# Performance work log

Measured on AMD Instinct MI355X. Metric: run time of the kernel, lower is better.

## Reference

```python
import jax, jax.numpy as jnp
import numpy as np

D = 2048          # lstm_size
V = 4096          # uniform num_tokens for all 5 decision groups
NUM_LAYERS = 4    # len(num_tokens) - 1 loop iterations; one final decode after


def setup_inputs() -> dict:
    key = jax.random.key(0)
    ks = jax.random.split(key, 10)
    s = 0.02
    n = lambda k, shape: jax.random.normal(k, shape, dtype=jnp.float32) * s
    return {
        "emb0": n(ks[0], (1, D)),                 # Embedding(1, D) initial input
        "w_ih": n(ks[1], (4 * D, D)),             # LSTMCell input weights (i,f,g,o)
        "w_hh": n(ks[2], (4 * D, D)),
        "b_ih": jnp.zeros((4 * D,), jnp.float32),
        "b_hh": jnp.zeros((4 * D,), jnp.float32),
        "lin1_w": n(ks[3], (D, D)),
        "lin1_b": jnp.zeros((D,), jnp.float32),
        "lin2_w": n(ks[4], (D, D)),
        "lin2_b": jnp.zeros((D,), jnp.float32),
        "lin3_w": n(ks[5], (1, D)),
        "lin3_b": jnp.zeros((1,), jnp.float32),
        "dec_w": n(ks[6], (5, V, D)),             # 5 decoders Linear(D, V)
        "dec_b": jnp.zeros((5, V), jnp.float32),
        "emb_tables": n(ks[7], (4, V, D)),        # only embeddings[0..3] are used
    }


def _lstm_cell(x, h, c, w_ih, w_hh, b_ih, b_hh):
    # torch.nn.LSTMCell math; gate order i, f, g, o
    gates = x @ w_ih.T + b_ih + h @ w_hh.T + b_hh
    i, f, g, o = jnp.split(gates, 4, axis=-1)
    i, f, o = jax.nn.sigmoid(i), jax.nn.sigmoid(f), jax.nn.sigmoid(o)
    g = jnp.tanh(g)
    c_new = f * c + i * g
    h_new = o * jnp.tanh(c_new)
    return h_new, c_new


def reference(emb0, w_ih, w_hh, b_ih, b_hh, lin1_w, lin1_b, lin2_w, lin2_b,
              lin3_w, lin3_b, dec_w, dec_b, emb_tables):
    key = jax.random.key(42)
    step = 0

    def sample(logits, step):
        # stable softmax stats computed once via log_softmax
        logp = jax.nn.log_softmax(logits, axis=-1)
        p = jnp.exp(logp)
        ent = -(logp * p).sum(1)                              # (1,)
        idx = jax.random.categorical(jax.random.fold_in(key, step), logits, axis=-1)  # (1,)
        sel_lp = jnp.take_along_axis(logp, idx[:, None], axis=1).squeeze(1)           # (1,)
        return idx, sel_lp, jax.lax.stop_gradient(ent)

    # NOTE: source names the LSTMCell outputs (next_c, next_h) = lstm(...),
    # i.e. swapped vs torch's (h, c). State threading stays consistent, but all
    # downstream linears/decoders/all_h consume the CELL state c. Reproduced here.
    h = jnp.zeros((1, D), jnp.float32)
    c = jnp.zeros((1, D), jnp.float32)
    inputs = emb0
    all_c, all_cw = [], []
    arc, lps, ents = [], [], []

    for layer_id in range(NUM_LAYERS):
        h, c = _lstm_cell(inputs, h, c, w_ih, w_hh, b_ih, b_hh)
        all_c.append(c)
        all_cw.append(c @ lin1_w.T + lin1_b)
        query = jnp.tanh((c @ lin2_w.T + lin2_b) + jnp.concatenate(all_cw, 0))  # (layer_id+1, D)
        logits = (query @ lin3_w.T + lin3_b).reshape(1, layer_id + 1)
        skip_idx, lp, en = sample(logits, step); step += 1
        arc.append(skip_idx); lps.append(lp); ents.append(en)
        inputs = jnp.concatenate(all_c, 0)[skip_idx]            # (1, D)

        h, c = _lstm_cell(inputs, h, c, w_ih, w_hh, b_ih, b_hh)
        logits = c @ dec_w[layer_id].T + dec_b[layer_id]        # (1, V)
        func, lp, en = sample(logits, step); step += 1
        arc.append(func); lps.append(lp); ents.append(en)
        inputs = emb_tables[layer_id][func]                     # (1, D)

    # final model decision
    h, c = _lstm_cell(inputs, h, c, w_ih, w_hh, b_ih, b_hh)
    logits = c @ dec_w[-1].T + dec_b[-1]
    func, lp, en = sample(logits, step)
    arc.append(func); lps.append(lp); ents.append(en)

    arc_seq = jnp.concatenate(arc, 0)            # (9,) int32
    sample_entropy = jnp.concatenate(ents, 0)    # (9,)
    sample_log_probs = jnp.concatenate(lps, 0)   # (9,)
    return arc_seq, sample_entropy, sample_log_probs
```

## Files before the change

kernel.cpp:

```cpp
#include <hip/hip_runtime.h>
#include <stdint.h>

#define D 2048
#define V 4096
#define TINYF 1.17549435e-38f
#define NINF (-__builtin_huge_valf())

#if __has_builtin(__builtin_amdgcn_cvt_pk_f32_fp8) && __has_builtin(__builtin_amdgcn_cvt_pk_fp8_f32)
#define HWFP8 1
#define POSTSCALE 0.015625f
#else
#define HWFP8 0
#define POSTSCALE 1.52587890625e-05f
#endif

typedef float vfloat2 __attribute__((ext_vector_type(2)));
typedef float vfloat4 __attribute__((ext_vector_type(4)));

__device__ __forceinline__ void tf_block(uint32_t k0, uint32_t k1, uint32_t x0, uint32_t x1,
                                         uint32_t& o0, uint32_t& o1) {
  uint32_t ks2 = k0 ^ k1 ^ 0x1BD11BDAu;
  uint32_t ks[3] = {k0, k1, ks2};
  x0 += k0; x1 += k1;
  const uint32_t rotA[4] = {13u, 15u, 26u, 6u};
  const uint32_t rotB[4] = {17u, 29u, 16u, 24u};
#pragma unroll
  for (int i = 0; i < 5; ++i) {
    const uint32_t* rot = (i & 1) ? rotB : rotA;
#pragma unroll
    for (int j = 0; j < 4; ++j) {
      uint32_t r = rot[j];
      x0 += x1;
      x1 = (x1 << r) | (x1 >> (32u - r));
      x1 ^= x0;
    }
    x0 += ks[(i + 1) % 3];
    x1 += ks[(i + 2) % 3] + (uint32_t)(i + 1);
  }
  o0 = x0; o1 = x1;
}

__device__ __forceinline__ float gumbel_at(uint32_t k1, uint32_t k2, int i) {
  uint32_t o0, o1;
  tf_block(k1, k2, 0u, (uint32_t)i, o0, o1);
  uint32_t bits = o0 ^ o1;
  float u = __uint_as_float((bits >> 9) | 0x3F800000u) - 1.0f;
  u = fmaxf(TINYF, u + TINYF);
  return -logf(-logf(u));
}

#if !HWFP8
__device__ __forceinline__ float dec1(uint32_t v) {
  uint32_t e = (v >> 3) & 15u, m = v & 7u;
  int K = e ? (int)((8u + m) << e) : (int)(m << 1);
  float f = (float)K;
  return (v & 0x80u) ? -f : f;
}
__device__ __forceinline__ uint32_t enc1(float xf) {
  uint32_t b = __float_as_uint(xf);
  uint32_t s = (b >> 24) & 0x80u;
  float ax = fabsf(xf);
  if (ax < 0.015625f) return s | (uint32_t)(int)rintf(ax * 512.f);
  uint32_t ab = b & 0x7FFFFFFFu;
  ab += 0x7FFFFu + ((ab >> 20) & 1u);
  int e = (int)(ab >> 23) - 120;
  uint32_t m = (ab >> 20) & 7u;
  if (e < 1) return s | (uint32_t)(int)rintf(ax * 512.f);
  if (e > 15) { e = 15; m = 7u; }
  return s | ((uint32_t)e << 3) | m;
}
#endif

__device__ __forceinline__ void dec8(uint2 u, float* w) {
#if HWFP8
  vfloat2 a = __builtin_amdgcn_cvt_pk_f32_fp8((int)u.x, false);
  vfloat2 b = __builtin_amdgcn_cvt_pk_f32_fp8((int)u.x, true);
  vfloat2 c = __builtin_amdgcn_cvt_pk_f32_fp8((int)u.y, false);
  vfloat2 d = __builtin_amdgcn_cvt_pk_f32_fp8((int)u.y, true);
  w[0] = a.x; w[1] = a.y; w[2] = b.x; w[3] = b.y;
  w[4] = c.x; w[5] = c.y; w[6] = d.x; w[7] = d.y;
#else
  uint32_t p = u.x, q = u.y;
  w[0] = dec1(p & 255u); w[1] = dec1((p >> 8) & 255u);
  w[2] = dec1((p >> 16) & 255u); w[3] = dec1(p >> 24);
  w[4] = dec1(q & 255u); w[5] = dec1((q >> 8) & 255u);
  w[6] = dec1((q >> 16) & 255u); w[7] = dec1(q >> 24);
#endif
}

__device__ __forceinline__ float4 ntload4(const float4* p) {
  vfloat4 v = __builtin_nontemporal_load((const vfloat4*)p);
  return make_float4(v.x, v.y, v.z, v.w);
}

__device__ __forceinline__ float row_dot8(const uint8_t* __restrict__ row,
                                          const float* __restrict__ xs, int lane) {
  float a = 0.f;
#pragma unroll
  for (int k = lane * 8; k < D; k += 512) {
    uint2 u = *(const uint2*)(row + k);
    float w[8]; dec8(u, w);
    float4 x0 = *(const float4*)(xs + k);
    float4 x1 = *(const float4*)(xs + k + 4);
    a += w[0] * x0.x + w[1] * x0.y + w[2] * x0.z + w[3] * x0.w
       + w[4] * x1.x + w[5] * x1.y + w[6] * x1.z + w[7] * x1.w;
  }
  return a;
}

__global__ __launch_bounds__(256) void convert_k(const float* __restrict__ wih,
                                                 const float* __restrict__ whh,
                                                 const float* __restrict__ l1,
                                                 const float* __restrict__ l2,
                                                 uint8_t* __restrict__ dw) {
  size_t gid = (size_t)blockIdx.x * 256 + threadIdx.x;
  const size_t C1 = (size_t)4 * D * D / 8;
  const size_t C2 = 2 * C1;
  const size_t C3 = C2 + (size_t)D * D / 8;
  const size_t C4 = C3 + (size_t)D * D / 8;
  const float* src; size_t off, dbase;
  if (gid < C1)      { src = wih; off = gid;      dbase = 0; }
  else if (gid < C2) { src = whh; off = gid - C1; dbase = (size_t)4 * D * D; }
  else if (gid < C3) { src = l1;  off = gid - C2; dbase = (size_t)8 * D * D; }
  else if (gid < C4) { src = l2;  off = gid - C3; dbase = (size_t)9 * D * D; }
  else return;
  const float4* s = (const float4*)(src + off * 8);
  float4 a = ntload4(s), b = ntload4(s + 1);
  float v[8] = {a.x * 64.f, a.y * 64.f, a.z * 64.f, a.w * 64.f,
                b.x * 64.f, b.y * 64.f, b.z * 64.f, b.w * 64.f};
  uint2 o;
#if HWFP8
  int lo = __builtin_amdgcn_cvt_pk_fp8_f32(v[0], v[1], 0, false);
  lo     = __builtin_amdgcn_cvt_pk_fp8_f32(v[2], v[3], lo, true);
  int hi = __builtin_amdgcn_cvt_pk_fp8_f32(v[4], v[5], 0, false);
  hi     = __builtin_amdgcn_cvt_pk_fp8_f32(v[6], v[7], hi, true);
  o.x = (uint32_t)lo; o.y = (uint32_t)hi;
#else
  o.x = enc1(v[0]) | (enc1(v[1]) << 8) | (enc1(v[2]) << 16) | (enc1(v[3]) << 24);
  o.y = enc1(v[4]) | (enc1(v[5]) << 8) | (enc1(v[6]) << 16) | (enc1(v[7]) << 24);
#endif
  *(uint2*)(dw + dbase + off * 8) = o;
}

template <bool SAMPLE>
__global__ __launch_bounds__(256) void lstm_cell_k(
    const uint8_t* __restrict__ w_ih, const uint8_t* __restrict__ w_hh,
    const float* __restrict__ b_ih, const float* __restrict__ b_hh,
    const float* __restrict__ x_base, const float* __restrict__ logits, int step,
    const float* __restrict__ h_in, const float* __restrict__ c_in,
    float* __restrict__ h_out, float* __restrict__ c_out, float* __restrict__ c_copy,
    float* __restrict__ out_arc, float* __restrict__ out_ent, float* __restrict__ out_lp) {
  __shared__ float xs[D];
  __shared__ float hs[D];
  __shared__ float red[256];
  __shared__ int redi[256];
  __shared__ int s_sel;
  int tid = threadIdx.x;
  const float* x = x_base;
  if (SAMPLE) {
    uint32_t k1, k2; tf_block(0u, 42u, 0u, (uint32_t)step, k1, k2);
    float xv[16];
    float m = NINF, bv = NINF; int bi = 1 << 30;
#pragma unroll
    for (int t = 0; t < 16; ++t) {
      int i = tid + t * 256;
      float xl = logits[i];
      xv[t] = xl;
      m = fmaxf(m, xl);
      float sc = gumbel_at(k1, k2, i) + xl;
      if (sc > bv) { bv = sc; bi = i; }
    }
    red[tid] = m; __syncthreads();
    for (int st = 128; st; st >>= 1) { if (tid < st) red[tid] = fmaxf(red[tid], red[tid + st]); __syncthreads(); }
    m = red[0]; __syncthreads();
    float S = 0.f, T = 0.f;
#pragma unroll
    for (int t = 0; t < 16; ++t) { float e = expf(xv[t] - m); S += e; T += e * (xv[t] - m); }
    red[tid] = S; __syncthreads();
    for (int st = 128; st; st >>= 1) { if (tid < st) red[tid] += red[tid + st]; __syncthreads(); }
    S = red[0]; __syncthreads();
    red[tid] = T; __syncthreads();
    for (int st = 128; st; st >>= 1) { if (tid < st) red[tid] += red[tid + st]; __syncthreads(); }
    T = red[0]; __syncthreads();
    red[tid] = bv; redi[tid] = bi; __syncthreads();
    for (int st = 128; st; st >>= 1) {
      if (tid < st) {
        float ov = red[tid + st]; int oi = redi[tid + st];
        if (ov > red[tid] || (ov == red[tid] && oi < redi[tid])) { red[tid] = ov; redi[tid] = oi; }
      }
      __syncthreads();
    }
    if (tid == 0) {
      int idx = redi[0];
      s_sel = idx;
      if (blockIdx.x == 0) {
        float L = logf(S);
        *out_arc = (float)idx;
        *out_ent = L - T / S;
        *out_lp  = logits[idx] - m - L;
      }
    }
    __syncthreads();
    x = x_base + (size_t)s_sel * D;
  }
  for (int i = tid; i < D; i += 256) { xs[i] = x[i]; hs[i] = h_in ? h_in[i] : 0.f; }
  __syncthreads();
  int wave = tid >> 6, lane = tid & 63;
  int j = blockIdx.x * 4 + wave;
  float gv[4];
#pragma unroll
  for (int m4 = 0; m4 < 4; ++m4) {
    float a = row_dot8(w_ih + (size_t)(m4 * D + j) * D, xs, lane)
            + row_dot8(w_hh + (size_t)(m4 * D + j) * D, hs, lane);
#pragma unroll
    for (int off = 32; off > 0; off >>= 1) a += __shfl_down(a, off, 64);
    gv[m4] = a * POSTSCALE + b_ih[m4 * D + j] + b_hh[m4 * D + j];
  }
  if (lane == 0) {
    float ig = 1.f / (1.f + expf(-gv[0]));
    float fg = 1.f / (1.f + expf(-gv[1]));
    float gg = tanhf(gv[2]);
    float og = 1.f / (1.f + expf(-gv[3]));
    float ci = c_in ? c_in[j] : 0.f;
    float cn = fg * ci + ig * gg;
    float hn = og * tanhf(cn);
    c_out[j] = cn;
    h_out[j] = hn;
    if (c_copy) c_copy[j] = cn;
  }
}

template <int NC>
__global__ __launch_bounds__(256) void spec_lin_k(
    const uint8_t* __restrict__ w_ih, const uint8_t* __restrict__ w_hh,
    const float* __restrict__ b_ih, const float* __restrict__ b_hh,
    const float* __restrict__ h1, const float* __restrict__ all_c,
    const uint8_t* __restrict__ l1w, const float* __restrict__ l1b,
    const uint8_t* __restrict__ l2w, const float* __restrict__ l2b,
    const float* __restrict__ c1,
    float* __restrict__ g_ih, float* __restrict__ g_hh,
    float* __restrict__ cw_dst, float* __restrict__ qb) {
  __shared__ float xs[D];
  int tid = threadIdx.x;
  int wave = tid >> 6, lane = tid & 63;
  int b = blockIdx.x;
  if (b < 512) {
    int j = b * 4 + wave;
    float acc[4][NC + 1];
#pragma unroll
    for (int m = 0; m < 4; ++m)
#pragma unroll
      for (int t = 0; t < NC + 1; ++t) acc[m][t] = 0.f;
    for (int k = lane * 8; k < D; k += 512) {
      float xh[8];
      float xc[NC][8];
      *(float4*)xh       = *(const float4*)(h1 + k);
      *(float4*)(xh + 4) = *(const float4*)(h1 + k + 4);
#pragma unroll
      for (int t = 0; t < NC; ++t) {
        *(float4*)(xc[t])     = *(const float4*)(all_c + (size_t)t * D + k);
        *(float4*)(xc[t] + 4) = *(const float4*)(all_c + (size_t)t * D + k + 4);
      }
#pragma unroll
      for (int m = 0; m < 4; ++m) {
        float wi[8], wh[8];
        dec8(*(const uint2*)(w_ih + (size_t)(m * D + j) * D + k), wi);
        dec8(*(const uint2*)(w_hh + (size_t)(m * D + j) * D + k), wh);
#pragma unroll
        for (int e = 0; e < 8; ++e) acc[m][0] += wh[e] * xh[e];
#pragma unroll
        for (int t = 0; t < NC; ++t)
#pragma unroll
          for (int e = 0; e < 8; ++e) acc[m][1 + t] += wi[e] * xc[t][e];
      }
    }
#pragma unroll
    for (int m = 0; m < 4; ++m)
#pragma unroll
      for (int t = 0; t < NC + 1; ++t) {
        float a = acc[m][t];
#pragma unroll
        for (int o = 32; o > 0; o >>= 1) a += __shfl_down(a, o, 64);
        if (lane == 0) {
          if (t == 0) g_hh[m * D + j] = a * POSTSCALE + b_ih[m * D + j] + b_hh[m * D + j];
          else        g_ih[((size_t)(t - 1) * 4 + m) * D + j] = a * POSTSCALE;
        }
      }
  } else {
    for (int i = tid; i < D; i += 256) xs[i] = c1[i];
    __syncthreads();
    int b2 = b - 512;
    const uint8_t* Wp; const float* bp; float* dst; int row;
    if (b2 < 512) { row = b2 * 4 + wave; Wp = l1w; bp = l1b; dst = cw_dst; }
    else          { row = (b2 - 512) * 4 + wave; Wp = l2w; bp = l2b; dst = qb; }
    float a = row_dot8(Wp + (size_t)row * D, xs, lane);
#pragma unroll
    for (int o = 32; o > 0; o >>= 1) a += __shfl_down(a, o, 64);
    if (lane == 0) dst[row] = a * POSTSCALE + bp[row];
  }
}

__global__ __launch_bounds__(256) void dec_fused_k(
    const float* __restrict__ Wdec, const float* __restrict__ bdec,
    const float* __restrict__ g_ih, const float* __restrict__ g_hh,
    const float* __restrict__ c1,
    const float* __restrict__ qb, const float* __restrict__ all_cw,
    const float* __restrict__ lin3_w, const float* __restrict__ lin3_b,
    int ncand, int step,
    float* __restrict__ logits,
    float* __restrict__ h2_out, float* __restrict__ c2_out,
    float* __restrict__ out_arc, float* __restrict__ out_ent, float* __restrict__ out_lp) {
  __shared__ float xs[D];
  __shared__ float red[16];
  __shared__ int s_sel;
  int tid = threadIdx.x, wave = tid >> 6, lane = tid & 63;
  for (int t = 0; t < ncand; ++t) {
    float s = 0.f;
    for (int k = tid; k < D; k += 256) s += tanhf(qb[k] + all_cw[(size_t)t * D + k]) * lin3_w[k];
#pragma unroll
    for (int o = 32; o > 0; o >>= 1) s += __shfl_down(s, o, 64);
    if (lane == 0) red[t * 4 + wave] = s;
  }
  __syncthreads();
  if (tid == 0) {
    float sl[4];
    for (int t = 0; t < ncand; ++t)
      sl[t] = red[t * 4] + red[t * 4 + 1] + red[t * 4 + 2] + red[t * 4 + 3] + lin3_b[0];
    uint32_t k1, k2; tf_block(0u, 42u, 0u, (uint32_t)step, k1, k2);
    float m = NINF;
    for (int i = 0; i < ncand; ++i) m = fmaxf(m, sl[i]);
    float S = 0.f, T = 0.f;
    for (int i = 0; i < ncand; ++i) { float e = expf(sl[i] - m); S += e; T += e * (sl[i] - m); }
    float L = logf(S);
    float bv = NINF; int bi = 0;
    for (int i = 0; i < ncand; ++i) {
      float sc = gumbel_at(k1, k2, i) + sl[i];
      if (sc > bv) { bv = sc; bi = i; }
    }
    s_sel = bi;
    if (blockIdx.x == 0) {
      *out_arc = (float)bi;
      *out_ent = L - T / S;
      *out_lp  = sl[bi] - m - L;
    }
  }
  __syncthreads();
  int sel = s_sel;
  const float* gi = g_ih + (size_t)sel * 4 * D;
  bool b0 = (blockIdx.x == 0);
  for (int j = tid; j < D; j += 256) {
    float gI = gi[j]         + g_hh[j];
    float gF = gi[D + j]     + g_hh[D + j];
    float gG = gi[2 * D + j] + g_hh[2 * D + j];
    float gO = gi[3 * D + j] + g_hh[3 * D + j];
    float ig = 1.f / (1.f + expf(-gI));
    float fg = 1.f / (1.f + expf(-gF));
    float gg = tanhf(gG);
    float og = 1.f / (1.f + expf(-gO));
    float cn = fg * c1[j] + ig * gg;
    xs[j] = cn;
    if (b0) { c2_out[j] = cn; h2_out[j] = og * tanhf(cn); }
  }
  __syncthreads();
  int row = blockIdx.x * 4 + wave;
  const float* wr = Wdec + (size_t)row * D;
  float a = 0.f;
#pragma unroll
  for (int k = lane * 4; k < D; k += 256) {
    float4 w = ntload4((const float4*)(wr + k));
    float4 x = *(const float4*)(xs + k);
    a += w.x * x.x + w.y * x.y + w.z * x.z + w.w * x.w;
  }
#pragma unroll
  for (int o = 32; o > 0; o >>= 1) a += __shfl_down(a, o, 64);
  if (lane == 0) logits[row] = a + bdec[row];
}

__global__ __launch_bounds__(256) void gemv_k(const float* __restrict__ W,
                                              const float* __restrict__ bias,
                                              const float* __restrict__ c,
                                              float* __restrict__ y) {
  __shared__ float xs[D];
  int tid = threadIdx.x;
  for (int i = tid; i < D; i += 256) xs[i] = c[i];
  __syncthreads();
  int wave = tid >> 6, lane = tid & 63;
  int row = blockIdx.x * 4 + wave;
  const float* wr = W + (size_t)row * D;
  float a = 0.f;
#pragma unroll
  for (int k = lane * 4; k < D; k += 256) {
    float4 w = ntload4((const float4*)(wr + k));
    float4 x = *(const float4*)(xs + k);
    a += w.x * x.x + w.y * x.y + w.z * x.z + w.w * x.w;
  }
#pragma unroll
  for (int o = 32; o > 0; o >>= 1) a += __shfl_down(a, o, 64);
  if (lane == 0) y[row] = a + bias[row];
}

__global__ __launch_bounds__(1024) void sample_k(const float* __restrict__ logits, int step,
                                                 float* __restrict__ out_arc,
                                                 float* __restrict__ out_ent,
                                                 float* __restrict__ out_lp,
                                                 int* __restrict__ sel_out) {
  __shared__ float red[1024];
  __shared__ int redi[1024];
  int tid = threadIdx.x;
  uint32_t k1, k2; tf_block(0u, 42u, 0u, (uint32_t)step, k1, k2);
  float xv[4];
  float m = NINF, bv = NINF; int bi = 1 << 30;
#pragma unroll
  for (int t = 0; t < 4; ++t) {
    int i = tid + t * 1024;
    float x = logits[i];
    xv[t] = x;
    m = fmaxf(m, x);
    float sc = gumbel_at(k1, k2, i) + x;
    if (sc > bv) { bv = sc; bi = i; }
  }
  red[tid] = m; __syncthreads();
  for (int st = 512; st; st >>= 1) { if (tid < st) red[tid] = fmaxf(red[tid], red[tid + st]); __syncthreads(); }
  m = red[0]; __syncthreads();
  float S = 0.f, T = 0.f;
#pragma unroll
  for (int t = 0; t < 4; ++t) { float e = expf(xv[t] - m); S += e; T += e * (xv[t] - m); }
  red[tid] = S; __syncthreads();
  for (int st = 512; st; st >>= 1) { if (tid < st) red[tid] += red[tid + st]; __syncthreads(); }
  S = red[0]; __syncthreads();
  red[tid] = T; __syncthreads();
  for (int st = 512; st; st >>= 1) { if (tid < st) red[tid] += red[tid + st]; __syncthreads(); }
  T = red[0]; __syncthreads();
  red[tid] = bv; redi[tid] = bi; __syncthreads();
  for (int st = 512; st; st >>= 1) {
    if (tid < st) {
      float ov = red[tid + st]; int oi = redi[tid + st];
      if (ov > red[tid] || (ov == red[tid] && oi < redi[tid])) { red[tid] = ov; redi[tid] = oi; }
    }
    __syncthreads();
  }
  if (tid == 0) {
    float L = logf(S);
    int idx = redi[0];
    *out_arc = (float)idx;
    *out_ent = L - T / S;
    *out_lp  = logits[idx] - m - L;
    *sel_out = idx;
  }
}

extern "C" void kernel_launch(void* const* d_in, const int* in_sizes, int n_in,
                              void* d_out, int out_size, void* d_ws, size_t ws_size,
                              hipStream_t stream) {
  const float* emb0   = (const float*)d_in[0];
  const float* w_ih   = (const float*)d_in[1];
  const float* w_hh   = (const float*)d_in[2];
  const float* b_ih   = (const float*)d_in[3];
  const float* b_hh   = (const float*)d_in[4];
  const float* lin1_w = (const float*)d_in[5];
  const float* lin1_b = (const float*)d_in[6];
  const float* lin2_w = (const float*)d_in[7];
  const float* lin2_b = (const float*)d_in[8];
  const float* lin3_w = (const float*)d_in[9];
  const float* lin3_b = (const float*)d_in[10];
  const float* dec_w  = (const float*)d_in[11];
  const float* dec_b  = (const float*)d_in[12];
  const float* embt   = (const float*)d_in[13];

  float* out = (float*)d_out;
  float* ws = (float*)d_ws;

  float* hA     = ws;
  float* cA     = ws + D;
  float* hB     = ws + 2 * D;
  float* cB     = ws + 3 * D;
  float* all_c  = ws + 4 * D;
  float* all_cw = ws + 8 * D;
  float* qb     = ws + 12 * D;
  float* logits = ws + 13 * D;
  int* sel_d    = (int*)(ws + 15 * D);
  float* g_hh   = ws + 16 * D;
  float* g_ih   = ws + 20 * D;
  uint8_t* w8   = (uint8_t*)(ws + 36 * D);
  uint8_t* wih8 = w8;
  uint8_t* whh8 = w8 + (size_t)4 * D * D;
  uint8_t* l18  = w8 + (size_t)8 * D * D;
  uint8_t* l28  = w8 + (size_t)9 * D * D;

  convert_k<<<20480, 256, 0, stream>>>(w_ih, w_hh, lin1_w, lin2_w, w8);

  auto launch_spec = [&](int layer) {
    float* cw = all_cw + (size_t)layer * D;
    switch (layer) {
      case 0:  spec_lin_k<1><<<1536, 256, 0, stream>>>(wih8, whh8, b_ih, b_hh, hA, all_c, l18, lin1_b, l28, lin2_b, cA, g_ih, g_hh, cw, qb); break;
      case 1:  spec_lin_k<2><<<1536, 256, 0, stream>>>(wih8, whh8, b_ih, b_hh, hA, all_c, l18, lin1_b, l28, lin2_b, cA, g_ih, g_hh, cw, qb); break;
      case 2:  spec_lin_k<3><<<1536, 256, 0, stream>>>(wih8, whh8, b_ih, b_hh, hA, all_c, l18, lin1_b, l28, lin2_b, cA, g_ih, g_hh, cw, qb); break;
      default: spec_lin_k<4><<<1536, 256, 0, stream>>>(wih8, whh8, b_ih, b_hh, hA, all_c, l18, lin1_b, l28, lin2_b, cA, g_ih, g_hh, cw, qb); break;
    }
  };

  for (int layer = 0; layer < 4; ++layer) {
    float* ccopy = all_c + (size_t)layer * D;
    if (layer == 0) {
      lstm_cell_k<false><<<512, 256, 0, stream>>>(wih8, whh8, b_ih, b_hh,
                                                  emb0, nullptr, 0,
                                                  nullptr, nullptr, hA, cA, ccopy,
                                                  nullptr, nullptr, nullptr);
    } else {
      int ps = 2 * layer - 1;
      lstm_cell_k<true><<<512, 256, 0, stream>>>(wih8, whh8, b_ih, b_hh,
                                                 embt + (size_t)(layer - 1) * V * D,
                                                 logits, ps,
                                                 hB, cB, hA, cA, ccopy,
                                                 out + ps, out + 9 + ps, out + 18 + ps);
    }
    launch_spec(layer);
    int step = 2 * layer;
    dec_fused_k<<<V / 4, 256, 0, stream>>>(dec_w + (size_t)layer * V * D,
                                           dec_b + (size_t)layer * V,
                                           g_ih, g_hh, cA, qb, all_cw, lin3_w, lin3_b,
                                           layer + 1, step, logits, hB, cB,
                                           out + step, out + 9 + step, out + 18 + step);
  }

  lstm_cell_k<true><<<512, 256, 0, stream>>>(wih8, whh8, b_ih, b_hh,
                                             embt + (size_t)3 * V * D, logits, 7,
                                             hB, cB, hA, cA, nullptr,
                                             out + 7, out + 16, out + 25);
  gemv_k<<<V / 4, 256, 0, stream>>>(dec_w + (size_t)4 * V * D, dec_b + (size_t)4 * V,
                                    cA, logits);
  sample_k<<<1, 1024, 0, stream>>>(logits, 8, out + 8, out + 17, out + 26, sel_d);
}
```

Baseline: 282.4 us.

## Fuse fp8 weight conversion into first use and precompute sampling partials

Drops the separate conversion kernel. The first LSTM cell and the first spec_lin pass now read the fp32 weights, compute the dot product in full precision, and write the fp8 copy as a side effect. The decoder GEMV kernels also emit per-block softmax/Gumbel partials (max, sum, entropy term, best score and index), so each sampling LSTM block and the final sampler only merge 1024 partials instead of rescanning all 4096 logits. This removes a full extra pass over the weights and repeated per-block Gumbel/exp work. The trade-off is that the first step uses fp32 weights, which differs numerically from the quantized path, and the partial merges use a rescaled online-softmax combine.

```diff
diff --git a/kernel.cpp b/kernel.cpp
--- a/kernel.cpp
+++ b/kernel.cpp
@@ -88,46 +88,7 @@
 #endif
 }
 
-__device__ __forceinline__ float4 ntload4(const float4* p) {
-  vfloat4 v = __builtin_nontemporal_load((const vfloat4*)p);
-  return make_float4(v.x, v.y, v.z, v.w);
-}
-
-__device__ __forceinline__ float row_dot8(const uint8_t* __restrict__ row,
-                                          const float* __restrict__ xs, int lane) {
-  float a = 0.f;
-#pragma unroll
-  for (int k = lane * 8; k < D; k += 512) {
-    uint2 u = *(const uint2*)(row + k);
-    float w[8]; dec8(u, w);
-    float4 x0 = *(const float4*)(xs + k);
-    float4 x1 = *(const float4*)(xs + k + 4);
-    a += w[0] * x0.x + w[1] * x0.y + w[2] * x0.z + w[3] * x0.w
-       + w[4] * x1.x + w[5] * x1.y + w[6] * x1.z + w[7] * x1.w;
-  }
-  return a;
-}
-
-__global__ __launch_bounds__(256) void convert_k(const float* __restrict__ wih,
-                                                 const float* __restrict__ whh,
-                                                 const float* __restrict__ l1,
-                                                 const float* __restrict__ l2,
-                                                 uint8_t* __restrict__ dw) {
-  size_t gid = (size_t)blockIdx.x * 256 + threadIdx.x;
-  const size_t C1 = (size_t)4 * D * D / 8;
-  const size_t C2 = 2 * C1;
-  const size_t C3 = C2 + (size_t)D * D / 8;
-  const size_t C4 = C3 + (size_t)D * D / 8;
-  const float* src; size_t off, dbase;
-  if (gid < C1)      { src = wih; off = gid;      dbase = 0; }
-  else if (gid < C2) { src = whh; off = gid - C1; dbase = (size_t)4 * D * D; }
-  else if (gid < C3) { src = l1;  off = gid - C2; dbase = (size_t)8 * D * D; }
-  else if (gid < C4) { src = l2;  off = gid - C3; dbase = (size_t)9 * D * D; }
-  else return;
-  const float4* s = (const float4*)(src + off * 8);
-  float4 a = ntload4(s), b = ntload4(s + 1);
-  float v[8] = {a.x * 64.f, a.y * 64.f, a.z * 64.f, a.w * 64.f,
-                b.x * 64.f, b.y * 64.f, b.z * 64.f, b.w * 64.f};
+__device__ __forceinline__ uint2 enc8(const float* v) {
   uint2 o;
 #if HWFP8
   int lo = __builtin_amdgcn_cvt_pk_fp8_f32(v[0], v[1], 0, false);
@@ -139,69 +100,130 @@
   o.x = enc1(v[0]) | (enc1(v[1]) << 8) | (enc1(v[2]) << 16) | (enc1(v[3]) << 24);
   o.y = enc1(v[4]) | (enc1(v[5]) << 8) | (enc1(v[6]) << 16) | (enc1(v[7]) << 24);
 #endif
-  *(uint2*)(dw + dbase + off * 8) = o;
-}
-
-template <bool SAMPLE>
+  return o;
+}
+
+__device__ __forceinline__ float4 ntload4(const float4* p) {
+  vfloat4 v = __builtin_nontemporal_load((const vfloat4*)p);
+  return make_float4(v.x, v.y, v.z, v.w);
+}
+
+__device__ __forceinline__ float row_dot8(const uint8_t* __restrict__ row,
+                                          const float* __restrict__ xs, int lane) {
+  float a = 0.f;
+#pragma unroll
+  for (int k = lane * 8; k < D; k += 512) {
+    uint2 u = *(const uint2*)(row + k);
+    float w[8]; dec8(u, w);
+    float4 x0 = *(const float4*)(xs + k);
+    float4 x1 = *(const float4*)(xs + k + 4);
+    a += w[0] * x0.x + w[1] * x0.y + w[2] * x0.z + w[3] * x0.w
+       + w[4] * x1.x + w[5] * x1.y + w[6] * x1.z + w[7] * x1.w;
+  }
+  return a;
+}
+
+__device__ __forceinline__ float row_dot_conv(const float* __restrict__ row,
+                                              const float* __restrict__ xs, int lane,
+                                              uint8_t* __restrict__ out8) {
+  float a = 0.f;
+#pragma unroll
+  for (int k = lane * 8; k < D; k += 512) {
+    float4 w0 = ntload4((const float4*)(row + k));
+    float4 w1 = ntload4((const float4*)(row + k + 4));
+    float4 x0 = *(const float4*)(xs + k);
+    float4 x1 = *(const float4*)(xs + k + 4);
+    a += w0.x * x0.x + w0.y * x0.y + w0.z * x0.z + w0.w * x0.w
+       + w1.x * x1.x + w1.y * x1.y + w1.z * x1.z + w1.w * x1.w;
+    float v[8] = {w0.x * 64.f, w0.y * 64.f, w0.z * 64.f, w0.w * 64.f,
+                  w1.x * 64.f, w1.y * 64.f, w1.z * 64.f, w1.w * 64.f};
+    *(uint2*)(out8 + k) = enc8(v);
+  }
+  return a;
+}
+
+struct SampPart { float m, S, T, bv; int bi; };
+
+__device__ __forceinline__ void merge_part(SampPart& a, float qm, float qS, float qT,
+                                           float qb, int qi) {
+  float nm = fmaxf(a.m, qm);
+  float ea = expf(a.m - nm), eq = expf(qm - nm);
+  a.T = (a.T + (a.m - nm) * a.S) * ea + (qT + (qm - nm) * qS) * eq;
+  a.S = a.S * ea + qS * eq;
+  a.m = nm;
+  if (qb > a.bv || (qb == a.bv && qi < a.bi)) { a.bv = qb; a.bi = qi; }
+}
+
+__device__ __forceinline__ SampPart reduce_parts(const float4* __restrict__ part4,
+                                                 const int* __restrict__ parti,
+                                                 float* rm, float* rS, float* rT,
+                                                 float* rb, int* ri, int tid) {
+  float4 p = part4[4 * tid];
+  SampPart a = {p.x, p.y, p.z, p.w, parti[4 * tid]};
+#pragma unroll
+  for (int r = 1; r < 4; ++r) {
+    float4 q = part4[4 * tid + r];
+    merge_part(a, q.x, q.y, q.z, q.w, parti[4 * tid + r]);
+  }
+  rm[tid] = a.m; rS[tid] = a.S; rT[tid] = a.T; rb[tid] = a.bv; ri[tid] = a.bi;
+  __syncthreads();
+  for (int st = 128; st; st >>= 1) {
+    if (tid < st) {
+      merge_part(a, rm[tid + st], rS[tid + st], rT[tid + st], rb[tid + st], ri[tid + st]);
+      rm[tid] = a.m; rS[tid] = a.S; rT[tid] = a.T; rb[tid] = a.bv; ri[tid] = a.bi;
+    }
+    __syncthreads();
+  }
+  SampPart res = {rm[0], rS[0], rT[0], rb[0], ri[0]};
+  __syncthreads();
+  return res;
+}
+
+__device__ __forceinline__ void block_partial(const float* sl4, int base, int step,
+                                              float4* __restrict__ part4,
+                                              int* __restrict__ parti, int blk) {
+  uint32_t k1, k2; tf_block(0u, 42u, 0u, (uint32_t)step, k1, k2);
+  float x0 = sl4[0], x1 = sl4[1], x2 = sl4[2], x3 = sl4[3];
+  float pm = fmaxf(fmaxf(x0, x1), fmaxf(x2, x3));
+  float e0 = expf(x0 - pm), e1 = expf(x1 - pm), e2 = expf(x2 - pm), e3 = expf(x3 - pm);
+  float pS = e0 + e1 + e2 + e3;
+  float pT = e0 * (x0 - pm) + e1 * (x1 - pm) + e2 * (x2 - pm) + e3 * (x3 - pm);
+  float pb = NINF; int pbi = base;
+  float g;
+  g = gumbel_at(k1, k2, base + 0) + x0; if (g > pb) { pb = g; pbi = base + 0; }
+  g = gumbel_at(k1, k2, base + 1) + x1; if (g > pb) { pb = g; pbi = base + 1; }
+  g = gumbel_at(k1, k2, base + 2) + x2; if (g > pb) { pb = g; pbi = base + 2; }
+  g = gumbel_at(k1, k2, base + 3) + x3; if (g > pb) { pb = g; pbi = base + 3; }
+  part4[blk] = make_float4(pm, pS, pT, pb);
+  parti[blk] = pbi;
+}
+
+template <bool CONV, bool SAMPLE>
 __global__ __launch_bounds__(256) void lstm_cell_k(
-    const uint8_t* __restrict__ w_ih, const uint8_t* __restrict__ w_hh,
+    const void* __restrict__ w_ih_v, const void* __restrict__ w_hh_v,
+    uint8_t* __restrict__ wih8_out, uint8_t* __restrict__ whh8_out,
     const float* __restrict__ b_ih, const float* __restrict__ b_hh,
-    const float* __restrict__ x_base, const float* __restrict__ logits, int step,
+    const float* __restrict__ x_base,
+    const float4* __restrict__ part4, const int* __restrict__ parti,
+    const float* __restrict__ logits,
     const float* __restrict__ h_in, const float* __restrict__ c_in,
     float* __restrict__ h_out, float* __restrict__ c_out, float* __restrict__ c_copy,
     float* __restrict__ out_arc, float* __restrict__ out_ent, float* __restrict__ out_lp) {
   __shared__ float xs[D];
   __shared__ float hs[D];
-  __shared__ float red[256];
-  __shared__ int redi[256];
-  __shared__ int s_sel;
+  __shared__ float rm[256], rS[256], rT[256], rb[256];
+  __shared__ int ri[256];
   int tid = threadIdx.x;
   const float* x = x_base;
   if (SAMPLE) {
-    uint32_t k1, k2; tf_block(0u, 42u, 0u, (uint32_t)step, k1, k2);
-    float xv[16];
-    float m = NINF, bv = NINF; int bi = 1 << 30;
-#pragma unroll
-    for (int t = 0; t < 16; ++t) {
-      int i = tid + t * 256;
-      float xl = logits[i];
-      xv[t] = xl;
-      m = fmaxf(m, xl);
-      float sc = gumbel_at(k1, k2, i) + xl;
-      if (sc > bv) { bv = sc; bi = i; }
-    }
-    red[tid] = m; __syncthreads();
-    for (int st = 128; st; st >>= 1) { if (tid < st) red[tid] = fmaxf(red[tid], red[tid + st]); __syncthreads(); }
-    m = red[0]; __syncthreads();
-    float S = 0.f, T = 0.f;
-#pragma unroll
-    for (int t = 0; t < 16; ++t) { float e = expf(xv[t] - m); S += e; T += e * (xv[t] - m); }
-    red[tid] = S; __syncthreads();
-    for (int st = 128; st; st >>= 1) { if (tid < st) red[tid] += red[tid + st]; __syncthreads(); }
-    S = red[0]; __syncthreads();
-    red[tid] = T; __syncthreads();
-    for (int st = 128; st; st >>= 1) { if (tid < st) red[tid] += red[tid + st]; __syncthreads(); }
-    T = red[0]; __syncthreads();
-    red[tid] = bv; redi[tid] = bi; __syncthreads();
-    for (int st = 128; st; st >>= 1) {
-      if (tid < st) {
-        float ov = red[tid + st]; int oi = redi[tid + st];
-        if (ov > red[tid] || (ov == red[tid] && oi < redi[tid])) { red[tid] = ov; redi[tid] = oi; }
-      }
-      __syncthreads();
-    }
-    if (tid == 0) {
-      int idx = redi[0];
-      s_sel = idx;
-      if (blockIdx.x == 0) {
-        float L = logf(S);
-        *out_arc = (float)idx;
-        *out_ent = L - T / S;
-        *out_lp  = logits[idx] - m - L;
-      }
-    }
-    __syncthreads();
-    x = x_base + (size_t)s_sel * D;
+    SampPart g = reduce_parts(part4, parti, rm, rS, rT, rb, ri, tid);
+    if (tid == 0 && blockIdx.x == 0) {
+      float L = logf(g.S);
+      *out_arc = (float)g.bi;
+      *out_ent = L - g.T / g.S;
+      *out_lp  = logits[g.bi] - g.m - L;
+    }
+    x = x_base + (size_t)g.bi * D;
   }
   for (int i = tid; i < D; i += 256) { xs[i] = x[i]; hs[i] = h_in ? h_in[i] : 0.f; }
   __syncthreads();
@@ -210,11 +232,19 @@
   float gv[4];
 #pragma unroll
   for (int m4 = 0; m4 < 4; ++m4) {
-    float a = row_dot8(w_ih + (size_t)(m4 * D + j) * D, xs, lane)
-            + row_dot8(w_hh + (size_t)(m4 * D + j) * D, hs, lane);
+    size_t roff = (size_t)(m4 * D + j) * D;
+    float a;
+    if (CONV) {
+      a = row_dot_conv((const float*)w_ih_v + roff, xs, lane, wih8_out + roff)
+        + row_dot_conv((const float*)w_hh_v + roff, hs, lane, whh8_out + roff);
+    } else {
+      a = row_dot8((const uint8_t*)w_ih_v + roff, xs, lane)
+        + row_dot8((const uint8_t*)w_hh_v + roff, hs, lane);
+      a *= POSTSCALE;
+    }
 #pragma unroll
     for (int off = 32; off > 0; off >>= 1) a += __shfl_down(a, off, 64);
-    gv[m4] = a * POSTSCALE + b_ih[m4 * D + j] + b_hh[m4 * D + j];
+    gv[m4] = a + b_ih[m4 * D + j] + b_hh[m4 * D + j];
   }
   if (lane == 0) {
     float ig = 1.f / (1.f + expf(-gv[0]));
@@ -230,13 +260,14 @@
   }
 }
 
-template <int NC>
+template <int NC, bool CONV>
 __global__ __launch_bounds__(256) void spec_lin_k(
     const uint8_t* __restrict__ w_ih, const uint8_t* __restrict__ w_hh,
     const float* __restrict__ b_ih, const float* __restrict__ b_hh,
     const float* __restrict__ h1, const float* __restrict__ all_c,
-    const uint8_t* __restrict__ l1w, const float* __restrict__ l1b,
-    const uint8_t* __restrict__ l2w, const float* __restrict__ l2b,
+    const void* __restrict__ l1_v, const float* __restrict__ l1b,
+    const void* __restrict__ l2_v, const float* __restrict__ l2b,
+    uint8_t* __restrict__ l18_out, uint8_t* __restrict__ l28_out,
     const float* __restrict__ c1,
     float* __restrict__ g_ih, float* __restrict__ g_hh,
     float* __restrict__ cw_dst, float* __restrict__ qb) {
@@ -290,13 +321,16 @@
     for (int i = tid; i < D; i += 256) xs[i] = c1[i];
     __syncthreads();
     int b2 = b - 512;
-    const uint8_t* Wp; const float* bp; float* dst; int row;
-    if (b2 < 512) { row = b2 * 4 + wave; Wp = l1w; bp = l1b; dst = cw_dst; }
-    else          { row = (b2 - 512) * 4 + wave; Wp = l2w; bp = l2b; dst = qb; }
-    float a = row_dot8(Wp + (size_t)row * D, xs, lane);
+    const void* Wp; const float* bp; float* dst; uint8_t* o8; int row;
+    if (b2 < 512) { row = b2 * 4 + wave; Wp = l1_v; bp = l1b; dst = cw_dst; o8 = l18_out; }
+    else          { row = (b2 - 512) * 4 + wave; Wp = l2_v; bp = l2b; dst = qb; o8 = l28_out; }
+    size_t roff = (size_t)row * D;
+    float a;
+    if (CONV) a = row_dot_conv((const float*)Wp + roff, xs, lane, o8 + roff);
+    else      a = row_dot8((const uint8_t*)Wp + roff, xs, lane) * POSTSCALE;
 #pragma unroll
     for (int o = 32; o > 0; o >>= 1) a += __shfl_down(a, o, 64);
-    if (lane == 0) dst[row] = a * POSTSCALE + bp[row];
+    if (lane == 0) dst[row] = a + bp[row];
   }
 }
 
@@ -309,9 +343,11 @@
     int ncand, int step,
     float* __restrict__ logits,
     float* __restrict__ h2_out, float* __restrict__ c2_out,
-    float* __restrict__ out_arc, float* __restrict__ out_ent, float* __restrict__ out_lp) {
+    float* __restrict__ out_arc, float* __restrict__ out_ent, float* __restrict__ out_lp,
+    float4* __restrict__ part4, int* __restrict__ parti) {
   __shared__ float xs[D];
   __shared__ float red[16];
+  __shared__ float sl4[4];
   __shared__ int s_sel;
   int tid = threadIdx.x, wave = tid >> 6, lane = tid & 63;
   for (int t = 0; t < ncand; ++t) {
@@ -373,14 +409,17 @@
   }
 #pragma unroll
   for (int o = 32; o > 0; o >>= 1) a += __shfl_down(a, o, 64);
-  if (lane == 0) logits[row] = a + bdec[row];
-}
-
-__global__ __launch_bounds__(256) void gemv_k(const float* __restrict__ W,
-                                              const float* __restrict__ bias,
-                                              const float* __restrict__ c,
-                                              float* __restrict__ y) {
+  if (lane == 0) { float lv = a + bdec[row]; logits[row] = lv; sl4[wave] = lv; }
+  __syncthreads();
+  if (tid == 0) block_partial(sl4, blockIdx.x * 4, step + 1, part4, parti, blockIdx.x);
+}
+
+__global__ __launch_bounds__(256) void gemv_k(
+    const float* __restrict__ W, const float* __restrict__ bias,
+    const float* __restrict__ c, float* __restrict__ y, int step,
+    float4* __restrict__ part4, int* __restrict__ parti) {
   __shared__ float xs[D];
+  __shared__ float sl4[4];
   int tid = threadIdx.x;
   for (int i = tid; i < D; i += 256) xs[i] = c[i];
   __syncthreads();
@@ -396,56 +435,24 @@
   }
 #pragma unroll
   for (int o = 32; o > 0; o >>= 1) a += __shfl_down(a, o, 64);
-  if (lane == 0) y[row] = a + bias[row];
-}
-
-__global__ __launch_bounds__(1024) void sample_k(const float* __restrict__ logits, int step,
-                                                 float* __restrict__ out_arc,
-                                                 float* __restrict__ out_ent,
-                                                 float* __restrict__ out_lp,
-                                                 int* __restrict__ sel_out) {
-  __shared__ float red[1024];
-  __shared__ int redi[1024];
+  if (lane == 0) { float lv = a + bias[row]; y[row] = lv; sl4[wave] = lv; }
+  __syncthreads();
+  if (tid == 0) block_partial(sl4, blockIdx.x * 4, step, part4, parti, blockIdx.x);
+}
+
+__global__ __launch_bounds__(256) void reduce_sample_k(
+    const float4* __restrict__ part4, const int* __restrict__ parti,
+    const float* __restrict__ logits,
+    float* __restrict__ out_arc, float* __restrict__ out_ent, float* __restrict__ out_lp) {
+  __shared__ float rm[256], rS[256], rT[256], rb[256];
+  __shared__ int ri[256];
   int tid = threadIdx.x;
-  uint32_t k1, k2; tf_block(0u, 42u, 0u, (uint32_t)step, k1, k2);
-  float xv[4];
-  float m = NINF, bv = NINF; int bi = 1 << 30;
-#pragma unroll
-  for (int t = 0; t < 4; ++t) {
-    int i = tid + t * 1024;
-    float x = logits[i];
-    xv[t] = x;
-    m = fmaxf(m, x);
-    float sc = gumbel_at(k1, k2, i) + x;
-    if (sc > bv) { bv = sc; bi = i; }
-  }
-  red[tid] = m; __syncthreads();
-  for (int st = 512; st; st >>= 1) { if (tid < st) red[tid] = fmaxf(red[tid], red[tid + st]); __syncthreads(); }
-  m = red[0]; __syncthreads();
-  float S = 0.f, T = 0.f;
-#pragma unroll
-  for (int t = 0; t < 4; ++t) { float e = expf(xv[t] - m); S += e; T += e * (xv[t] - m); }
-  red[tid] = S; __syncthreads();
-  for (int st = 512; st; st >>= 1) { if (tid < st) red[tid] += red[tid + st]; __syncthreads(); }
-  S = red[0]; __syncthreads();
-  red[tid] = T; __syncthreads();
-  for (int st = 512; st; st >>= 1) { if (tid < st) red[tid] += red[tid + st]; __syncthreads(); }
-  T = red[0]; __syncthreads();
-  red[tid] = bv; redi[tid] = bi; __syncthreads();
-  for (int st = 512; st; st >>= 1) {
-    if (tid < st) {
-      float ov = red[tid + st]; int oi = redi[tid + st];
-      if (ov > red[tid] || (ov == red[tid] && oi < redi[tid])) { red[tid] = ov; redi[tid] = oi; }
-    }
-    __syncthreads();
-  }
+  SampPart g = reduce_parts(part4, parti, rm, rS, rT, rb, ri, tid);
   if (tid == 0) {
-    float L = logf(S);
-    int idx = redi[0];
-    *out_arc = (float)idx;
-    *out_ent = L - T / S;
-    *out_lp  = logits[idx] - m - L;
-    *sel_out = idx;
+    float L = logf(g.S);
+    *out_arc = (float)g.bi;
+    *out_ent = L - g.T / g.S;
+    *out_lp  = logits[g.bi] - g.m - L;
   }
 }
 
@@ -478,56 +485,58 @@
   float* all_cw = ws + 8 * D;
   float* qb     = ws + 12 * D;
   float* logits = ws + 13 * D;
-  int* sel_d    = (int*)(ws + 15 * D);
-  float* g_hh   = ws + 16 * D;
-  float* g_ih   = ws + 20 * D;
-  uint8_t* w8   = (uint8_t*)(ws + 36 * D);
+  float* g_hh   = ws + 15 * D;
+  float* g_ih   = ws + 19 * D;
+  float4* part4 = (float4*)(ws + 36 * D);
+  int* parti    = (int*)(ws + 38 * D);
+  uint8_t* w8   = (uint8_t*)(ws + 40 * D);
   uint8_t* wih8 = w8;
   uint8_t* whh8 = w8 + (size_t)4 * D * D;
   uint8_t* l18  = w8 + (size_t)8 * D * D;
   uint8_t* l28  = w8 + (size_t)9 * D * D;
 
-  convert_k<<<20480, 256, 0, stream>>>(w_ih, w_hh, lin1_w, lin2_w, w8);
-
-  auto launch_spec = [&](int layer) {
-    float* cw = all_cw + (size_t)layer * D;
-    switch (layer) {
-      case 0:  spec_lin_k<1><<<1536, 256, 0, stream>>>(wih8, whh8, b_ih, b_hh, hA, all_c, l18, lin1_b, l28, lin2_b, cA, g_ih, g_hh, cw, qb); break;
-      case 1:  spec_lin_k<2><<<1536, 256, 0, stream>>>(wih8, whh8, b_ih, b_hh, hA, all_c, l18, lin1_b, l28, lin2_b, cA, g_ih, g_hh, cw, qb); break;
-      case 2:  spec_lin_k<3><<<1536, 256, 0, stream>>>(wih8, whh8, b_ih, b_hh, hA, all_c, l18, lin1_b, l28, lin2_b, cA, g_ih, g_hh, cw, qb); break;
-      default: spec_lin_k<4><<<1536, 256, 0, stream>>>(wih8, whh8, b_ih, b_hh, hA, all_c, l18, lin1_b, l28, lin2_b, cA, g_ih, g_hh, cw, qb); break;
-    }
-  };
-
   for (int layer = 0; layer < 4; ++layer) {
     float* ccopy = all_c + (size_t)layer * D;
     if (layer == 0) {
-      lstm_cell_k<false><<<512, 256, 0, stream>>>(wih8, whh8, b_ih, b_hh,
-                                                  emb0, nullptr, 0,
-                                                  nullptr, nullptr, hA, cA, ccopy,
-                                                  nullptr, nullptr, nullptr);
+      lstm_cell_k<true, false><<<512, 256, 0, stream>>>(
+          w_ih, w_hh, wih8, whh8, b_ih, b_hh, emb0,
+          nullptr, nullptr, nullptr, nullptr, nullptr,
+          hA, cA, ccopy, nullptr, nullptr, nullptr);
     } else {
       int ps = 2 * layer - 1;
-      lstm_cell_k<true><<<512, 256, 0, stream>>>(wih8, whh8, b_ih, b_hh,
-                                                 embt + (size_t)(layer - 1) * V * D,
-                                                 logits, ps,
-                                                 hB, cB, hA, cA, ccopy,
-                                                 out + ps, out + 9 + ps, out + 18 + ps);
-    }
-    launch_spec(layer);
+      lstm_cell_k<false, true><<<512, 256, 0, stream>>>(
+          wih8, whh8, nullptr, nullptr, b_ih, b_hh,
+          embt + (size_t)(layer - 1) * V * D,
+          part4, parti, logits, hB, cB,
+          hA, cA, ccopy, out + ps, out + 9 + ps, out + 18 + ps);
+    }
+    float* cw = all_cw + (size_t)layer * D;
+    if (layer == 0) {
+      spec_lin_k<1, true><<<1536, 256, 0, stream>>>(
+          wih8, whh8, b_ih, b_hh, hA, all_c,
+          lin1_w, lin1_b, lin2_w, lin2_b, l18, l28,
+          cA, g_ih, g_hh, cw, qb);
+    } else {
+      switch (layer) {
+        case 1:  spec_lin_k<2, false><<<1536, 256, 0, stream>>>(wih8, whh8, b_ih, b_hh, hA, all_c, l18, lin1_b, l28, lin2_b, nullptr, nullptr, cA, g_ih, g_hh, cw, qb); break;
+        case 2:  spec_lin_k<3, false><<<1536, 256, 0, stream>>>(wih8, whh8, b_ih, b_hh, hA, all_c, l18, lin1_b, l28, lin2_b, nullptr, nullptr, cA, g_ih, g_hh, cw, qb); break;
+        default: spec_lin_k<4, false><<<1536, 256, 0, stream>>>(wih8, whh8, b_ih, b_hh, hA, all_c, l18, lin1_b, l28, lin2_b, nullptr, nullptr, cA, g_ih, g_hh, cw, qb); break;
+      }
+    }
     int step = 2 * layer;
     dec_fused_k<<<V / 4, 256, 0, stream>>>(dec_w + (size_t)layer * V * D,
                                            dec_b + (size_t)layer * V,
                                            g_ih, g_hh, cA, qb, all_cw, lin3_w, lin3_b,
                                            layer + 1, step, logits, hB, cB,
-                                           out + step, out + 9 + step, out + 18 + step);
-  }
-
-  lstm_cell_k<true><<<512, 256, 0, stream>>>(wih8, whh8, b_ih, b_hh,
-                                             embt + (size_t)3 * V * D, logits, 7,
-                                             hB, cB, hA, cA, nullptr,
-                                             out + 7, out + 16, out + 25);
+                                           out + step, out + 9 + step, out + 18 + step,
+                                           part4, parti);
+  }
+
+  lstm_cell_k<false, true><<<512, 256, 0, stream>>>(
+      wih8, whh8, nullptr, nullptr, b_ih, b_hh,
+      embt + (size_t)3 * V * D, part4, parti, logits, hB, cB,
+      hA, cA, nullptr, out + 7, out + 16, out + 25);
   gemv_k<<<V / 4, 256, 0, stream>>>(dec_w + (size_t)4 * V * D, dec_b + (size_t)4 * V,
-                                    cA, logits);
-  sample_k<<<1, 1024, 0, stream>>>(logits, 8, out + 8, out + 17, out + 26, sel_d);
-}
+                                    cA, logits, 8, part4, parti);
+  reduce_sample_k<<<1, 256, 0, stream>>>(part4, parti, logits, out + 8, out + 17, out + 26);
+}
```

After: 265.8 us. -5.9%, faster.
